# Kernel optimization log

Hardware: AMD Instinct MI355X
Metric: run time of the kernel (lower is better)

## Reference

```python
import jax, jax.numpy as jnp
import numpy as np

P1, P2, M1, M2, W_SEARCH, STEP = 7, 7, 18, 55, 37, 4
EPS = 1e-6  # F.pairwise_distance eps


def align_corners(x, s, value):
    N, C, H, W = x.shape
    i = (s - H % s + 1) % s
    j = (s - W % s + 1) % s
    x = jnp.pad(x, ((0, 0), (0, 0), (0, i), (0, j)), constant_values=value)
    rows = jnp.array([H - 1, H - 1 + i]); cols = jnp.arange(0, W - 1, s)
    sub = x[:, :, rows[:, None], cols[None, :]]
    x = x.at[:, :, rows[:, None], cols[None, :]].set(sub[:, :, ::-1, :])
    rws = jnp.arange(0, H - 1, s); cls = jnp.array([W - 1, W - 1 + j])
    sub = x[:, :, rws[:, None], cls[None, :]]
    x = x.at[:, :, rws[:, None], cls[None, :]].set(sub[:, :, :, ::-1])
    rr = jnp.array([H - 1, H - 1 + i]); cc = jnp.array([W - 1, W - 1 + j])
    sub = x[:, :, rr, cc]
    x = x.at[:, :, rr, cc].set(sub[:, :, ::-1])
    return x


def unfold(x, p):  # torch F.unfold ordering: (N, C*p*p, (H-p+1)*(W-p+1))
    N, C, H, W = x.shape
    Hp, Wp = H - p + 1, W - p + 1
    cols = jnp.stack([x[:, :, ki:ki + Hp, kj:kj + Wp] for ki in range(p) for kj in range(p)], axis=2)
    return cols.reshape(N, C * p * p, Hp * Wp)


def fold(cols, H, W, p, C):  # torch F.fold: overlap-add
    N = cols.shape[0]; Hp, Wp = H - p + 1, W - p + 1
    cols = cols.reshape(N, C, p, p, Hp, Wp)
    out = jnp.zeros((N, C, H, W), cols.dtype)
    for ki in range(p):
        for kj in range(p):
            out = out.at[:, :, ki:ki + Hp, kj:kj + Wp].add(cols[:, :, ki, kj])
    return out


def block_matching(x, m, p, w, s):
    v = w // 2
    N, C, H, W = x.shape
    patches = unfold(x, p).reshape(N, C * p * p, H - p + 1, W - p + 1)
    patches = align_corners(patches, s, jnp.inf)
    _, d, k, l = patches.shape
    ref = patches[:, :, ::s, ::s].transpose(0, 2, 3, 1)                # (N,K,L,d)
    pad = jnp.pad(patches, ((0, 0), (0, 0), (v, v), (v, v)), constant_values=jnp.inf).transpose(0, 2, 3, 1)
    K, L = ref.shape[1], ref.shape[2]
    col_idx = jnp.arange(w)[:, None] + s * jnp.arange(L)[None, :]      # (w,L)
    dists = []
    for i in range(w):  # fixed-size search-window loop (hyperparameter)
        pad_i = pad[:, i:i + k:s, :, :]                                # (N,K,l+2v,d)
        g = pad_i[:, :, col_idx, :]                                    # (N,K,w,L,d)
        diff = g - ref[:, :, None, :, :] + EPS
        dists.append(jnp.sqrt(jnp.sum(diff * diff, axis=-1)))         # (N,K,w,L)
    dist = jnp.stack(dists, axis=2)                                    # (N,K,wi,wj,L)
    dist = dist.transpose(0, 1, 4, 2, 3).reshape(N, K, L, w * w)
    dist = dist.at[:, :, :, v * w + v].set(-jnp.inf)                   # force self-match
    idx = jax.lax.top_k(-dist, m)[1]                                   # (N,K,L,m) smallest distances
    ind_row = idx // w - v
    ind_col = idx % w - v
    row_ref = align_corners(jnp.arange(H - p + 1).reshape(1, 1, -1, 1), s, 0)[0, 0, ::s, 0]
    col_ref = align_corners(jnp.arange(W - p + 1).reshape(1, 1, 1, -1), s, 0)[0, 0, 0, ::s]
    ir = jnp.minimum(row_ref[None, :, None, None] + ind_row, H - p)
    ic = jnp.minimum(col_ref[None, None, :, None] + ind_col, W - p)
    return (ir * (W - p + 1) + ic).reshape(N, -1)                      # (N, K*L*m), block-major then m


def group_patches(y, indices, m, p):
    N, C, H, W = y.shape
    n = C * p * p
    unf = unfold(y, p)
    g = jnp.take_along_axis(unf, jnp.broadcast_to(indices[:, None, :], (N, n, indices.shape[1])), axis=2)
    return g.transpose(0, 2, 1).reshape(N, -1, m, n)                   # (N,B,m,n)


def denoise1(Y, sigma):
    N, B, m, n = Y.shape
    YtY = jnp.einsum('nbik,nbjk->nbij', Y, Y)
    Lc = jnp.linalg.cholesky(YtY)
    rhs = YtY - n * sigma ** 2 * jnp.eye(m, dtype=Y.dtype)
    theta = jax.scipy.linalg.cho_solve((Lc, True), rhs)
    X_hat = jnp.einsum('nbij,nbjk->nbik', theta, Y)
    wts = 1.0 / jnp.clip(jnp.sum(theta ** 2, axis=3, keepdims=True), 1.0 / m, 1.0)
    return X_hat, wts


def denoise2(Y, X, sigma):
    N, B, m, n = Y.shape
    XtX = jnp.einsum('nbik,nbjk->nbij', X, X)
    Lc = jnp.linalg.cholesky(XtX + n * sigma ** 2 * jnp.eye(m, dtype=Y.dtype))
    theta = jax.scipy.linalg.cho_solve((Lc, True), XtX)
    X_hat = jnp.einsum('nbij,nbjk->nbik', theta, Y)
    wts = 1.0 / jnp.clip(jnp.sum(theta ** 2, axis=3, keepdims=True), 1.0 / m, 1.0)
    return X_hat, wts


def aggregation(X_hat, wts, indices, size, p):
    N, C, H, W = size
    n = C * p * p
    Ltot = (H - p + 1) * (W - p + 1)
    Xc = (X_hat * wts).transpose(0, 3, 1, 2).reshape(N, n, -1)         # (N,n,B*m)
    wc = jnp.broadcast_to(wts.reshape(N, 1, -1), Xc.shape)

    def scat(cols, idx):
        return jnp.zeros((n, Ltot), cols.dtype).at[:, idx].add(cols)

    Xs = jax.vmap(scat)(Xc, indices)
    Ws = jax.vmap(scat)(wc, indices)
    return fold(Xs, H, W, p, C) / fold(Ws, H, W, p, C)


def nlridge(input_y, sigma):
    # step 1: noisy self-similarity + ridge with known sigma
    y_mean = jnp.mean(input_y, axis=1, keepdims=True)
    idx1 = block_matching(jax.lax.stop_gradient(y_mean), M1, P1, W_SEARCH, STEP)
    Y1 = group_patches(input_y, idx1, M1, P1)
    X1, w1 = denoise1(Y1, sigma)
    den1 = aggregation(X1, w1, idx1, input_y.shape, P1)
    # step 2: pilot-guided matching + ridge
    x_mean = jnp.mean(den1, axis=1, keepdims=True)
    idx2 = block_matching(jax.lax.stop_gradient(x_mean), M2, P2, W_SEARCH, STEP)
    Y2 = group_patches(input_y, idx2, M2, P2)
    X2 = group_patches(den1, idx2, M2, P2)
    Xh, w2 = denoise2(Y2, X2, sigma)
    return aggregation(Xh, w2, idx2, input_y.shape, P2)


def setup_inputs() -> dict:
    key = jax.random.key(0)
    input_y = jax.random.uniform(key, (2, 1, 256, 256), dtype=jnp.float32)
    sigma = jnp.array([0.1], dtype=jnp.float32)  # ~25/255 noise level
    return {'input_y': input_y, 'sigma': sigma}


def reference(input_y, sigma):
    return nlridge(input_y, sigma)
```

## Files before the change

kernel.cpp:

```cpp
#include <hip/hip_runtime.h>
#include <math.h>

#define IMG_H 256
#define IMG_W 256
#define IMG_SZ (IMG_H * IMG_W)
#define NP 49
#define HP 250
#define NPAT 62500
#define NB 4096
#define NCAND 1369
#define VRAD 18
#define CENTER (VRAD * 37 + VRAD)
#define NIMG 2
#define YSTR 52
#define WSTR 55

__device__ __forceinline__ bool align_map(int r, int c, int& ro, int& co) {
    if (r < 0 || r > 252 || c < 0 || c > 252) return false;
    if (r == 252) {
        if (c == 252) { ro = 249; co = 249; return true; }
        if (c <= 248 && (c & 3) == 0) { ro = 249; co = c; return true; }
        return false;
    }
    if (c == 252) {
        if (r <= 248 && (r & 3) == 0) { ro = r; co = 249; return true; }
        return false;
    }
    if (r >= 250 || c >= 250) return false;
    if (r == 249) {
        if (c == 249) return false;
        if ((c & 3) == 0) return false;
        ro = 249; co = c; return true;
    }
    if (c == 249) {
        if ((r & 3) == 0) return false;
        ro = r; co = 249; return true;
    }
    ro = r; co = c; return true;
}

__global__ void zero_kernel(float* __restrict__ p, int total) {
    int i = blockIdx.x * blockDim.x + threadIdx.x;
    if (i < total) p[i] = 0.0f;
}

__global__ void div_kernel(const float* __restrict__ acc, float* __restrict__ out, int total) {
    int i = blockIdx.x * blockDim.x + threadIdx.x;
    if (i < total) out[i] = acc[2 * i] / acc[2 * i + 1];
}

__global__ __launch_bounds__(256) void fold_div_kernel(const float* __restrict__ Xacc,
                                                       const float* __restrict__ Wacc,
                                                       float* __restrict__ out) {
    int e = blockIdx.x * 256 + threadIdx.x;
    if (e >= NIMG * IMG_SZ) return;
    int n = e / IMG_SZ, pix = e % IMG_SZ;
    int r = pix / IMG_W, c = pix % IMG_W;
    const float* Xn = Xacc + (size_t)n * NPAT * NP;
    const float* Wn = Wacc + (size_t)n * NPAT;
    float num = 0.f, den = 0.f;
#pragma unroll
    for (int ki = 0; ki < 7; ++ki) {
        int pr = r - ki;
        if (pr < 0 || pr > HP - 1) continue;
#pragma unroll
        for (int kj = 0; kj < 7; ++kj) {
            int pc = c - kj;
            if (pc < 0 || pc > HP - 1) continue;
            int p = pr * HP + pc;
            num += Xn[(size_t)p * NP + ki * 7 + kj];
            den += Wn[p];
        }
    }
    out[e] = num / den;
}

template <int M>
__global__ __launch_bounds__(256) void bm_kernel(const float* __restrict__ img,
                                                 int* __restrict__ idx_out) {
    __shared__ float win[43 * WSTR];
    __shared__ float dist[4][NCAND];
    const int llb = blockIdx.x, kk = blockIdx.y, n = blockIdx.z;
    const float* im = img + (size_t)n * IMG_SZ;
    const int t = threadIdx.x;
    const int w = t >> 6, lane = t & 63;
    const int ll = 4 * llb + w;
    const int rr = (kk < 63) ? 4 * kk : 249;
    const int cc = (ll < 63) ? 4 * ll : 249;
    const int ar0 = 4 * kk, ac0 = 4 * ll;
    const int acb = 16 * llb;
    const int row0 = max(0, ar0 - VRAD), col0 = max(0, acb - VRAD);
    const int row1 = min(IMG_H - 1, ar0 + VRAD + 6);
    const int col1 = min(IMG_W - 1, acb + 12 + VRAD + 6);
    const int nr = row1 - row0 + 1, nc = col1 - col0 + 1;
    for (int e = t; e < nr * nc; e += 256) {
        int r = e / nc, c = e % nc;
        win[r * WSTR + c] = im[(row0 + r) * IMG_W + col0 + c];
    }
    __syncthreads();
    float rf[NP];
    {
        const float* rb = &win[(rr - row0) * WSTR + (cc - col0)];
#pragma unroll
        for (int ki = 0; ki < 7; ++ki)
#pragma unroll
            for (int kj = 0; kj < 7; ++kj) rf[ki * 7 + kj] = rb[ki * WSTR + kj];
    }
    float* dw = dist[w];
    for (int cand = lane; cand < NCAND; cand += 64) {
        const int dr = cand / 37 - VRAD, dc = cand % 37 - VRAD;
        int ro, co;
        float d;
        if (align_map(ar0 + dr, ac0 + dc, ro, co)) {
            const float* base = &win[(ro - row0) * WSTR + (co - col0)];
            float s = 0.f;
#pragma unroll
            for (int ki = 0; ki < 7; ++ki)
#pragma unroll
                for (int kj = 0; kj < 7; ++kj) {
                    float df = base[ki * WSTR + kj] - rf[ki * 7 + kj] + 1e-6f;
                    s = fmaf(df, df, s);
                }
            d = sqrtf(s);
        } else {
            d = INFINITY;
        }
        if (cand == CENTER) d = -1.0f;
        dw[cand] = d;
    }
    __syncthreads();
    float v1 = INFINITY, v2 = INFINITY;
    int i1 = NCAND, i2 = NCAND;
    for (int c = lane; c < NCAND; c += 64) {
        float v = dw[c];
        if (v < v1) { v2 = v1; i2 = i1; v1 = v; i1 = c; }
        else if (v < v2) { v2 = v; i2 = c; }
    }
    int* out = idx_out + (size_t)((n * 64 + kk) * 64 + ll) * M;
    for (int sel = 0; sel < M; ++sel) {
        float gv = v1;
        int gi = i1;
#pragma unroll
        for (int off = 32; off; off >>= 1) {
            float vv = __shfl_xor(gv, off);
            int ii = __shfl_xor(gi, off);
            if (vv < gv || (vv == gv && ii < gi)) { gv = vv; gi = ii; }
        }
        if (lane == 0) {
            int dr = gi / 37 - VRAD, dc = gi % 37 - VRAD;
            out[sel] = min(rr + dr, 249) * HP + min(cc + dc, 249);
        }
        if ((gi & 63) == lane) {
            dw[gi] = INFINITY;
            v1 = v2; i1 = i2; v2 = INFINITY; i2 = NCAND;
            if (i1 == NCAND) {
                for (int c = lane; c < NCAND; c += 64) {
                    float v = dw[c];
                    if (v < v1) { v2 = v1; i2 = i1; v1 = v; i1 = c; }
                    else if (v < v2) { v2 = v; i2 = c; }
                }
            }
        }
    }
}

template <int M, bool R2, bool AGGP>
__global__ __launch_bounds__(128, 2) void denoise_kernel(
    const float* __restrict__ y, const float* __restrict__ xsrc,
    const int* __restrict__ idx, const float* __restrict__ sigma_p,
    float* __restrict__ accPix, float* __restrict__ Xacc, float* __restrict__ Wacc) {
    constexpr int PADM = (M + 3) & ~3;
    constexpr int PD = PADM + 4;
    constexpr int TPK = M * (M + 1) / 2;
    constexpr int NS = (TPK + 127) / 128;
    constexpr int NCH = PADM / 4;
    __shared__ __align__(16) float Ys[M][YSTR];
    __shared__ __align__(16) float SB[PADM * PD];
    __shared__ float cbuf[64];
    __shared__ __align__(16) float rdiag[PADM];
    __shared__ float wsh[M];
    __shared__ int gix[M];
    const int b = blockIdx.x, n = blockIdx.y;
    const int t = threadIdx.x;
    const int lane = t & 63, wv = t >> 6;
    if (t < M) gix[t] = idx[(size_t)(n * NB + b) * M + t];
    __syncthreads();
    const float* im = y + (size_t)n * IMG_SZ;
    const float* xim = xsrc + (size_t)n * IMG_SZ;
    for (int e = t; e < M * YSTR; e += 128) {
        int i = e / YSTR, ch = e - i * YSTR;
        int p = gix[i];
        float v = 0.f, vx = 0.f;
        if (ch < NP) {
            int off = (p / HP + ch / 7) * IMG_W + (p % HP + ch % 7);
            v = im[off];
            if (R2) vx = xim[off];
        }
        Ys[i][ch] = v;
        if (R2) SB[i * PD + ch] = vx;
    }
    __syncthreads();
    const float sg = sigma_p[0];
    const float cns = 49.f * sg * sg;
    int siR[NS], sjR[NS];
    float gsum[NS];
#pragma unroll
    for (int s = 0; s < NS; ++s) {
        int e = t + 128 * s;
        if (e < TPK) {
            int i = (int)((sqrtf(8.f * e + 1.f) - 1.f) * 0.5f);
            while ((i + 1) * (i + 2) / 2 <= e) ++i;
            while (i * (i + 1) / 2 > e) --i;
            siR[s] = i;
            sjR[s] = e - i * (i + 1) / 2;
        } else {
            siR[s] = -1;
            sjR[s] = 0;
        }
    }
#pragma unroll
    for (int s = 0; s < NS; ++s) {
        float sum = 0.f;
        if (siR[s] >= 0) {
            const float* Pi = R2 ? &SB[siR[s] * PD] : &Ys[siR[s]][0];
            const float* Pj = R2 ? &SB[sjR[s] * PD] : &Ys[sjR[s]][0];
#pragma unroll
            for (int q = 0; q < 13; ++q) {
                float4 a = *(const float4*)(Pi + 4 * q);
                float4 c4 = *(const float4*)(Pj + 4 * q);
                sum = fmaf(a.x, c4.x, sum);
                sum = fmaf(a.y, c4.y, sum);
                sum = fmaf(a.z, c4.z, sum);
                sum = fmaf(a.w, c4.w, sum);
            }
            if (R2 && siR[s] == sjR[s]) sum += cns;
        }
        gsum[s] = sum;
    }
    __syncthreads();
#pragma unroll
    for (int s = 0; s < NS; ++s)
        if (siR[s] >= 0) {
            SB[siR[s] * PD + sjR[s]] = gsum[s];
            SB[sjR[s] * PD + siR[s]] = gsum[s];
        }
    __syncthreads();
    if (wv == 0) {
        float g[PADM];
        const int ri = (lane < M) ? lane : 0;
#pragma unroll
        for (int jb = 0; jb < NCH; ++jb) {
            float4 v4 = *(const float4*)&SB[ri * PD + 4 * jb];
            g[4 * jb] = v4.x; g[4 * jb + 1] = v4.y; g[4 * jb + 2] = v4.z; g[4 * jb + 3] = v4.w;
        }
        if (lane >= M) {
#pragma unroll
            for (int j = 0; j < PADM; ++j) g[j] = (j == lane) ? 1.f : 0.f;
        }
#pragma unroll
        for (int k = 0; k < PADM - 1; ++k) {
            cbuf[lane] = g[k];
            float ivd = 1.f / cbuf[k];
            float fk = g[k] * ivd;
#pragma unroll
            for (int jb = (k + 1) / 4; jb < NCH; ++jb) {
                float4 cv = *(const float4*)&cbuf[4 * jb];
                if (4 * jb + 0 > k) g[4 * jb + 0] = fmaf(-fk, cv.x, g[4 * jb + 0]);
                if (4 * jb + 1 > k) g[4 * jb + 1] = fmaf(-fk, cv.y, g[4 * jb + 1]);
                if (4 * jb + 2 > k) g[4 * jb + 2] = fmaf(-fk, cv.z, g[4 * jb + 2]);
                if (4 * jb + 3 > k) g[4 * jb + 3] = fmaf(-fk, cv.w, g[4 * jb + 3]);
            }
        }
        if (lane < PADM) rdiag[lane] = (lane < M) ? 1.f / sqrtf(g[lane]) : 1.f;
        if (lane < PADM) {
#pragma unroll
            for (int jb = 0; jb < NCH; ++jb) {
                float4 rd = *(const float4*)&rdiag[4 * jb];
                float4 o;
                o.x = g[4 * jb] * rd.x; o.y = g[4 * jb + 1] * rd.y;
                o.z = g[4 * jb + 2] * rd.z; o.w = g[4 * jb + 3] * rd.w;
                *(float4*)&SB[lane * PD + 4 * jb] = o;
            }
        }
    }
    __syncthreads();
    const bool isId = (wv == 0) && (lane < M);
    const bool isY = (wv == 1) && (lane < NP);
    const int ch = (wv == 1 && lane < NP) ? lane : 0;
    float bb[PADM];
    if (wv == 1) {
#pragma unroll
        for (int i = 0; i < PADM; ++i) bb[i] = (i < M) ? Ys[i][ch] : 0.f;
    } else {
#pragma unroll
        for (int i = 0; i < PADM; ++i) bb[i] = (i == lane) ? 1.f : 0.f;
    }
#pragma unroll
    for (int ck = 0; ck < NCH; ++ck) {
        const int i0 = 4 * ck;
        float L10 = SB[(i0 + 1) * PD + i0];
        float L20 = SB[(i0 + 2) * PD + i0], L21 = SB[(i0 + 2) * PD + i0 + 1];
        float L30 = SB[(i0 + 3) * PD + i0], L31 = SB[(i0 + 3) * PD + i0 + 1],
              L32 = SB[(i0 + 3) * PD + i0 + 2];
        float b0 = bb[i0] * rdiag[i0];
        float b1 = (bb[i0 + 1] - L10 * b0) * rdiag[i0 + 1];
        float b2 = (bb[i0 + 2] - L20 * b0 - L21 * b1) * rdiag[i0 + 2];
        float b3 = (bb[i0 + 3] - L30 * b0 - L31 * b1 - L32 * b2) * rdiag[i0 + 3];
        bb[i0] = b0; bb[i0 + 1] = b1; bb[i0 + 2] = b2; bb[i0 + 3] = b3;
#pragma unroll
        for (int j = i0 + 4; j < PADM; ++j) {
            float4 L4 = *(const float4*)&SB[j * PD + i0];
            bb[j] = fmaf(-L4.x, b0, fmaf(-L4.y, b1, fmaf(-L4.z, b2, fmaf(-L4.w, b3, bb[j]))));
        }
        asm volatile("" ::: "memory");
    }
#pragma unroll
    for (int i = PADM - 1; i >= 0; --i) {
        float bbi = bb[i] * rdiag[i];
        bb[i] = bbi;
#pragma unroll
        for (int qb = 0; qb < i / 4; ++qb) {
            float4 L4 = *(const float4*)&SB[i * PD + 4 * qb];
            bb[4 * qb + 0] = fmaf(-L4.x, bbi, bb[4 * qb + 0]);
            bb[4 * qb + 1] = fmaf(-L4.y, bbi, bb[4 * qb + 1]);
            bb[4 * qb + 2] = fmaf(-L4.z, bbi, bb[4 * qb + 2]);
            bb[4 * qb + 3] = fmaf(-L4.w, bbi, bb[4 * qb + 3]);
        }
#pragma unroll
        for (int j = i & ~3; j < i; ++j)
            bb[j] = fmaf(-SB[i * PD + j], bbi, bb[j]);
        if ((i & 3) == 0) asm volatile("" ::: "memory");
    }
    float wloc = 0.f;
    if (isId) {
        float s2 = 0.f;
#pragma unroll
        for (int i = 0; i < M; ++i) {
            float th = ((i == lane) ? 1.f : 0.f) - cns * bb[i];
            s2 = fmaf(th, th, s2);
        }
        s2 = fminf(fmaxf(s2, 1.f / (float)M), 1.f);
        wloc = 1.f / s2;
        wsh[lane] = wloc;
    }
    if (!AGGP && isY) {
#pragma unroll
        for (int i = 0; i < M; ++i) Ys[i][ch] = fmaf(-cns, bb[i], Ys[i][ch]);
    }
    __syncthreads();
    if (AGGP) {
        if (isId) atomicAdd(&Wacc[(size_t)n * NPAT + gix[lane]], wloc);
        if (isY) {
#pragma unroll
            for (int i = 0; i < M; ++i) {
                float xv = fmaf(-cns, bb[i], Ys[i][ch]);
                atomicAdd(&Xacc[((size_t)n * NPAT + gix[i]) * NP + ch], xv * wsh[i]);
            }
        }
    } else {
        float* aA = accPix + (size_t)n * IMG_SZ * 2;
        for (int e = t; e < M * NP; e += 128) {
            int i = e / NP, c2 = e % NP;
            int p = gix[i];
            int pix = (p / HP + c2 / 7) * IMG_W + (p % HP + c2 % 7);
            float wi = wsh[i];
            atomicAdd(&aA[pix * 2], Ys[i][c2] * wi);
            atomicAdd(&aA[pix * 2 + 1], wi);
        }
    }
}

extern "C" void kernel_launch(void* const* d_in, const int* in_sizes, int n_in,
                              void* d_out, int out_size, void* d_ws, size_t ws_size,
                              hipStream_t stream) {
    const float* y = (const float*)d_in[0];
    const float* sigma = (const float*)d_in[1];
    float* out = (float*)d_out;

    char* ws = (char*)d_ws;
    size_t off = 0;
    auto carve = [&](size_t bytes) {
        void* p = ws + off;
        off += (bytes + 255) & ~(size_t)255;
        return p;
    };
    int* idx1 = (int*)carve((size_t)NIMG * NB * 18 * sizeof(int));
    int* idx2 = (int*)carve((size_t)NIMG * NB * 55 * sizeof(int));
    float* accPix = (float*)carve((size_t)NIMG * IMG_SZ * 2 * sizeof(float));
    float* den1 = (float*)carve((size_t)NIMG * IMG_SZ * sizeof(float));
    const size_t xw_floats = (size_t)NIMG * NPAT * (NP + 1);
    float* Xacc = (float*)carve(xw_floats * sizeof(float));
    float* Wacc = Xacc + (size_t)NIMG * NPAT * NP;
    const bool patchMode = (off <= ws_size);

    const int imgTotal = NIMG * IMG_SZ;

    if (patchMode) {
        const int xwTotal = (int)xw_floats;
        zero_kernel<<<(xwTotal + 255) / 256, 256, 0, stream>>>(Xacc, xwTotal);
        bm_kernel<18><<<dim3(16, 64, NIMG), 256, 0, stream>>>(y, idx1);
        denoise_kernel<18, false, true><<<dim3(NB, NIMG), 128, 0, stream>>>(
            y, y, idx1, sigma, accPix, Xacc, Wacc);
        fold_div_kernel<<<(imgTotal + 255) / 256, 256, 0, stream>>>(Xacc, Wacc, den1);
        zero_kernel<<<(xwTotal + 255) / 256, 256, 0, stream>>>(Xacc, xwTotal);
        bm_kernel<55><<<dim3(16, 64, NIMG), 256, 0, stream>>>(den1, idx2);
        denoise_kernel<55, true, true><<<dim3(NB, NIMG), 128, 0, stream>>>(
            y, den1, idx2, sigma, accPix, Xacc, Wacc);
        fold_div_kernel<<<(imgTotal + 255) / 256, 256, 0, stream>>>(Xacc, Wacc, out);
    } else {
        const int accTotal = NIMG * IMG_SZ * 2;
        zero_kernel<<<(accTotal + 255) / 256, 256, 0, stream>>>(accPix, accTotal);
        bm_kernel<18><<<dim3(16, 64, NIMG), 256, 0, stream>>>(y, idx1);
        denoise_kernel<18, false, false><<<dim3(NB, NIMG), 128, 0, stream>>>(
            y, y, idx1, sigma, accPix, Xacc, Wacc);
        div_kernel<<<(imgTotal + 255) / 256, 256, 0, stream>>>(accPix, den1, imgTotal);
        zero_kernel<<<(accTotal + 255) / 256, 256, 0, stream>>>(accPix, accTotal);
        bm_kernel<55><<<dim3(16, 64, NIMG), 256, 0, stream>>>(den1, idx2);
        denoise_kernel<55, true, false><<<dim3(NB, NIMG), 128, 0, stream>>>(
            y, den1, idx2, sigma, accPix, Xacc, Wacc);
        div_kernel<<<(imgTotal + 255) / 256, 256, 0, stream>>>(accPix, out, imgTotal);
    }
}
```

Before: 979.3 us.

## Pack Gram/Cholesky factor into lower-triangular shared layout and reuse buffer for Y

Replaces the square padded Gram/Cholesky shared buffer with a packed lower-triangular layout, indexed by a constexpr row-offset function that keeps 4-aligned chunks for float4 reads. The X patches for step 2 are loaded into the start of a single union buffer, and Y is loaded after the Gram is computed so both share the allocation. This lowers LDS footprint per block, which may allow more resident blocks for M=55. It also relaxes some compiler memory barriers. The cost is more complex indexing and a second pass of global loads for Y in the R2 path.

```diff
diff --git a/kernel.cpp b/kernel.cpp
--- a/kernel.cpp
+++ b/kernel.cpp
@@ -170,12 +170,15 @@
     const int* __restrict__ idx, const float* __restrict__ sigma_p,
     float* __restrict__ accPix, float* __restrict__ Xacc, float* __restrict__ Wacc) {
     constexpr int PADM = (M + 3) & ~3;
-    constexpr int PD = PADM + 4;
+    constexpr int NCH = PADM / 4;
     constexpr int TPK = M * (M + 1) / 2;
     constexpr int NS = (TPK + 127) / 128;
-    constexpr int NCH = PADM / 4;
-    __shared__ __align__(16) float Ys[M][YSTR];
-    __shared__ __align__(16) float SB[PADM * PD];
+    struct RO { static constexpr int f(int i) {
+        int a = i >> 2, b = i & 3; return 8 * a * (a + 1) + 4 * (a + 1) * b; } };
+    constexpr int LSZ = RO::f(PADM);
+    constexpr int YOFF = LSZ;
+    constexpr int UN = LSZ + M * YSTR;
+    __shared__ __align__(16) float SU[UN];
     __shared__ float cbuf[64];
     __shared__ __align__(16) float rdiag[PADM];
     __shared__ float wsh[M];
@@ -187,17 +190,18 @@
     __syncthreads();
     const float* im = y + (size_t)n * IMG_SZ;
     const float* xim = xsrc + (size_t)n * IMG_SZ;
-    for (int e = t; e < M * YSTR; e += 128) {
-        int i = e / YSTR, ch = e - i * YSTR;
-        int p = gix[i];
-        float v = 0.f, vx = 0.f;
-        if (ch < NP) {
-            int off = (p / HP + ch / 7) * IMG_W + (p % HP + ch % 7);
-            v = im[off];
-            if (R2) vx = xim[off];
-        }
-        Ys[i][ch] = v;
-        if (R2) SB[i * PD + ch] = vx;
+    {
+        const float* src = R2 ? xim : im;
+        float* dst = R2 ? &SU[0] : &SU[YOFF];
+        for (int e = t; e < M * YSTR; e += 128) {
+            int i = e / YSTR, ch = e - i * YSTR;
+            float v = 0.f;
+            if (ch < NP) {
+                int p = gix[i];
+                v = src[(p / HP + ch / 7) * IMG_W + (p % HP + ch % 7)];
+            }
+            dst[i * YSTR + ch] = v;
+        }
     }
     __syncthreads();
     const float sg = sigma_p[0];
@@ -218,42 +222,53 @@
             sjR[s] = 0;
         }
     }
-#pragma unroll
-    for (int s = 0; s < NS; ++s) {
-        float sum = 0.f;
-        if (siR[s] >= 0) {
-            const float* Pi = R2 ? &SB[siR[s] * PD] : &Ys[siR[s]][0];
-            const float* Pj = R2 ? &SB[sjR[s] * PD] : &Ys[sjR[s]][0];
-#pragma unroll
-            for (int q = 0; q < 13; ++q) {
-                float4 a = *(const float4*)(Pi + 4 * q);
-                float4 c4 = *(const float4*)(Pj + 4 * q);
-                sum = fmaf(a.x, c4.x, sum);
-                sum = fmaf(a.y, c4.y, sum);
-                sum = fmaf(a.z, c4.z, sum);
-                sum = fmaf(a.w, c4.w, sum);
-            }
-            if (R2 && siR[s] == sjR[s]) sum += cns;
-        }
-        gsum[s] = sum;
+    {
+        const float* base = R2 ? &SU[0] : &SU[YOFF];
+#pragma unroll
+        for (int s = 0; s < NS; ++s) {
+            float sum = 0.f;
+            if (siR[s] >= 0) {
+                const float* Pi = base + siR[s] * YSTR;
+                const float* Pj = base + sjR[s] * YSTR;
+#pragma unroll
+                for (int q = 0; q < 13; ++q) {
+                    float4 a = *(const float4*)(Pi + 4 * q);
+                    float4 c4 = *(const float4*)(Pj + 4 * q);
+                    sum = fmaf(a.x, c4.x, sum);
+                    sum = fmaf(a.y, c4.y, sum);
+                    sum = fmaf(a.z, c4.z, sum);
+                    sum = fmaf(a.w, c4.w, sum);
+                }
+                if (R2 && siR[s] == sjR[s]) sum += cns;
+            }
+            gsum[s] = sum;
+        }
     }
     __syncthreads();
 #pragma unroll
     for (int s = 0; s < NS; ++s)
-        if (siR[s] >= 0) {
-            SB[siR[s] * PD + sjR[s]] = gsum[s];
-            SB[sjR[s] * PD + siR[s]] = gsum[s];
-        }
+        if (siR[s] >= 0) SU[RO::f(siR[s]) + sjR[s]] = gsum[s];
+    if (R2) {
+        for (int e = t; e < M * YSTR; e += 128) {
+            int i = e / YSTR, ch = e - i * YSTR;
+            float v = 0.f;
+            if (ch < NP) {
+                int p = gix[i];
+                v = im[(p / HP + ch / 7) * IMG_W + (p % HP + ch % 7)];
+            }
+            SU[YOFF + i * YSTR + ch] = v;
+        }
+    }
     __syncthreads();
     if (wv == 0) {
         float g[PADM];
-        const int ri = (lane < M) ? lane : 0;
-#pragma unroll
-        for (int jb = 0; jb < NCH; ++jb) {
-            float4 v4 = *(const float4*)&SB[ri * PD + 4 * jb];
-            g[4 * jb] = v4.x; g[4 * jb + 1] = v4.y; g[4 * jb + 2] = v4.z; g[4 * jb + 3] = v4.w;
-        }
-        if (lane >= M) {
+        if (lane < M) {
+#pragma unroll
+            for (int j = 0; j < PADM; ++j) {
+                if (j >= M) g[j] = 0.f;
+                else g[j] = (j <= lane) ? SU[RO::f(lane) + j] : SU[RO::f(j) + lane];
+            }
+        } else {
 #pragma unroll
             for (int j = 0; j < PADM; ++j) g[j] = (j == lane) ? 1.f : 0.f;
         }
@@ -275,11 +290,15 @@
         if (lane < PADM) {
 #pragma unroll
             for (int jb = 0; jb < NCH; ++jb) {
-                float4 rd = *(const float4*)&rdiag[4 * jb];
-                float4 o;
-                o.x = g[4 * jb] * rd.x; o.y = g[4 * jb + 1] * rd.y;
-                o.z = g[4 * jb + 2] * rd.z; o.w = g[4 * jb + 3] * rd.w;
-                *(float4*)&SB[lane * PD + 4 * jb] = o;
+                if (4 * jb <= lane) {
+                    float4 rd4 = *(const float4*)&rdiag[4 * jb];
+                    float4 o;
+                    o.x = g[4 * jb + 0] * rd4.x;
+                    o.y = g[4 * jb + 1] * rd4.y;
+                    o.z = g[4 * jb + 2] * rd4.z;
+                    o.w = g[4 * jb + 3] * rd4.w;
+                    *(float4*)&SU[RO::f(lane) + 4 * jb] = o;
+                }
             }
         }
     }
@@ -290,7 +309,7 @@
     float bb[PADM];
     if (wv == 1) {
 #pragma unroll
-        for (int i = 0; i < PADM; ++i) bb[i] = (i < M) ? Ys[i][ch] : 0.f;
+        for (int i = 0; i < PADM; ++i) bb[i] = (i < M) ? SU[YOFF + i * YSTR + ch] : 0.f;
     } else {
 #pragma unroll
         for (int i = 0; i < PADM; ++i) bb[i] = (i == lane) ? 1.f : 0.f;
@@ -298,21 +317,21 @@
 #pragma unroll
     for (int ck = 0; ck < NCH; ++ck) {
         const int i0 = 4 * ck;
-        float L10 = SB[(i0 + 1) * PD + i0];
-        float L20 = SB[(i0 + 2) * PD + i0], L21 = SB[(i0 + 2) * PD + i0 + 1];
-        float L30 = SB[(i0 + 3) * PD + i0], L31 = SB[(i0 + 3) * PD + i0 + 1],
-              L32 = SB[(i0 + 3) * PD + i0 + 2];
+        float L10 = SU[RO::f(4 * ck + 1) + 4 * ck];
+        float L20 = SU[RO::f(4 * ck + 2) + 4 * ck], L21 = SU[RO::f(4 * ck + 2) + 4 * ck + 1];
+        float L30 = SU[RO::f(4 * ck + 3) + 4 * ck], L31 = SU[RO::f(4 * ck + 3) + 4 * ck + 1],
+              L32 = SU[RO::f(4 * ck + 3) + 4 * ck + 2];
         float b0 = bb[i0] * rdiag[i0];
         float b1 = (bb[i0 + 1] - L10 * b0) * rdiag[i0 + 1];
         float b2 = (bb[i0 + 2] - L20 * b0 - L21 * b1) * rdiag[i0 + 2];
         float b3 = (bb[i0 + 3] - L30 * b0 - L31 * b1 - L32 * b2) * rdiag[i0 + 3];
         bb[i0] = b0; bb[i0 + 1] = b1; bb[i0 + 2] = b2; bb[i0 + 3] = b3;
 #pragma unroll
-        for (int j = i0 + 4; j < PADM; ++j) {
-            float4 L4 = *(const float4*)&SB[j * PD + i0];
+        for (int j = 4 * ck + 4; j < PADM; ++j) {
+            float4 L4 = *(const float4*)&SU[RO::f(j) + 4 * ck];
             bb[j] = fmaf(-L4.x, b0, fmaf(-L4.y, b1, fmaf(-L4.z, b2, fmaf(-L4.w, b3, bb[j]))));
         }
-        asm volatile("" ::: "memory");
+        if (ck & 1) asm volatile("" ::: "memory");
     }
 #pragma unroll
     for (int i = PADM - 1; i >= 0; --i) {
@@ -320,7 +339,7 @@
         bb[i] = bbi;
 #pragma unroll
         for (int qb = 0; qb < i / 4; ++qb) {
-            float4 L4 = *(const float4*)&SB[i * PD + 4 * qb];
+            float4 L4 = *(const float4*)&SU[RO::f(i) + 4 * qb];
             bb[4 * qb + 0] = fmaf(-L4.x, bbi, bb[4 * qb + 0]);
             bb[4 * qb + 1] = fmaf(-L4.y, bbi, bb[4 * qb + 1]);
             bb[4 * qb + 2] = fmaf(-L4.z, bbi, bb[4 * qb + 2]);
@@ -328,8 +347,8 @@
         }
 #pragma unroll
         for (int j = i & ~3; j < i; ++j)
-            bb[j] = fmaf(-SB[i * PD + j], bbi, bb[j]);
-        if ((i & 3) == 0) asm volatile("" ::: "memory");
+            bb[j] = fmaf(-SU[RO::f(i) + j], bbi, bb[j]);
+        if ((i & 7) == 0) asm volatile("" ::: "memory");
     }
     float wloc = 0.f;
     if (isId) {
@@ -345,7 +364,8 @@
     }
     if (!AGGP && isY) {
 #pragma unroll
-        for (int i = 0; i < M; ++i) Ys[i][ch] = fmaf(-cns, bb[i], Ys[i][ch]);
+        for (int i = 0; i < M; ++i)
+            SU[YOFF + i * YSTR + ch] = fmaf(-cns, bb[i], SU[YOFF + i * YSTR + ch]);
     }
     __syncthreads();
     if (AGGP) {
@@ -353,7 +373,7 @@
         if (isY) {
 #pragma unroll
             for (int i = 0; i < M; ++i) {
-                float xv = fmaf(-cns, bb[i], Ys[i][ch]);
+                float xv = fmaf(-cns, bb[i], SU[YOFF + i * YSTR + ch]);
                 atomicAdd(&Xacc[((size_t)n * NPAT + gix[i]) * NP + ch], xv * wsh[i]);
             }
         }
@@ -364,7 +384,7 @@
             int p = gix[i];
             int pix = (p / HP + c2 / 7) * IMG_W + (p % HP + c2 % 7);
             float wi = wsh[i];
-            atomicAdd(&aA[pix * 2], Ys[i][c2] * wi);
+            atomicAdd(&aA[pix * 2], SU[YOFF + i * YSTR + c2] * wi);
             atomicAdd(&aA[pix * 2 + 1], wi);
         }
     }
```

After: 960.6 us. About the same (-1.9%).
